# Optimization experiments

Hardware: AMD Instinct MI355X
Metric: run time of the kernel (lower is better)

Reference implementation:

```python
import jax, jax.numpy as jnp
import numpy as np

MARGIN = 0.2
NEG_INF = -1e9  # safe stand-in for -inf when masking the max


def setup_inputs() -> dict:
    key = jax.random.key(0)
    k1, k2, k3 = jax.random.split(key, 3)
    B, D = 8192, 256
    p = jax.random.normal(k1, (B, D), dtype=jnp.float32)
    # module docstring says projections are normalized
    projections = p / jnp.linalg.norm(p, axis=1, keepdims=True)
    affordance_ids = jax.random.randint(k2, (B,), 0, 36, dtype=jnp.int64)
    instance_ids = jax.random.randint(k3, (B,), 0, 2048, dtype=jnp.int64)
    return {
        "projections": projections,
        "affordance_ids": affordance_ids,
        "instance_ids": instance_ids,
    }


def reference(projections, affordance_ids, instance_ids):
    # (B, B) cosine similarities
    sim = jnp.matmul(projections, projections.T)

    aff_eq = affordance_ids[:, None] == affordance_ids[None, :]
    inst_eq = instance_ids[:, None] == instance_ids[None, :]
    pos_mask = aff_eq & ~inst_eq          # same affordance, different instance
    neg_mask = ~aff_eq                    # different affordance

    # per-row hard negative: max similarity over negatives
    hard_neg = jnp.max(jnp.where(neg_mask, sim, NEG_INF), axis=1)  # (B,)

    # rows contribute only if they have >=1 positive AND >=1 negative
    valid_row = pos_mask.any(axis=1) & neg_mask.any(axis=1)        # (B,)
    pair_mask = pos_mask & valid_row[:, None]                      # (B, B)

    # margin loss for every (anchor i, positive j) pair
    losses = jnp.maximum(hard_neg[:, None] - sim + MARGIN, 0.0)

    total = jnp.sum(jnp.where(pair_mask, losses, 0.0))
    num_pairs = jnp.sum(pair_mask)
    return jnp.where(num_pairs > 0, total / num_pairs, 0.0)
```

## Files before the change

kernel.cpp:

```cpp
#include <hip/hip_runtime.h>

#define NB 8192
#define ND 256
#define NCLS 64
#define LOSS_MARGIN 0.2f
#define NEG_INF_F (-1e9f)
#define LMAXT 3
#define NBLK_LOSS (NCLS * LMAXT * LMAXT)
#define NTILE_T 2080

typedef __attribute__((ext_vector_type(8))) __bf16 bf16x8;
typedef __attribute__((ext_vector_type(4))) float f32x4;

__device__ __forceinline__ unsigned f2u_mono(float f) {
  unsigned b = __float_as_uint(f);
  return (b & 0x80000000u) ? ~b : (b | 0x80000000u);
}
__device__ __forceinline__ float u2f_mono(unsigned u) {
  return (u & 0x80000000u) ? __uint_as_float(u & 0x7fffffffu)
                           : __uint_as_float(~u);
}

__device__ __forceinline__ unsigned short f2bf(float f) {
  unsigned u = __float_as_uint(f);
  unsigned r = (u + 0x7fffu + ((u >> 16) & 1u)) >> 16;
  return (unsigned short)r;
}

__device__ __forceinline__ void gl_lds16(const void* gsrc, void* ldst) {
  __builtin_amdgcn_global_load_lds(
      (const __attribute__((address_space(1))) void*)gsrc,
      (__attribute__((address_space(3))) void*)ldst, 16, 0, 0);
}

__global__ __launch_bounds__(1024) void build_idx_fused(const int* __restrict__ aff,
                                                        int* __restrict__ class_start,
                                                        int* __restrict__ class_idx) {
  const int c = blockIdx.x;
  const int t = threadIdx.x;
  const int lane = t & 63, wave = t >> 6;
  __shared__ int wtot[16];
  __shared__ int s_off;

  int lt = 0;
  for (int i = t; i < NB; i += 1024) lt += (aff[i] < c) ? 1 : 0;
  for (int off = 32; off; off >>= 1) lt += __shfl_down(lt, off);
  if (lane == 0) wtot[wave] = lt;
  __syncthreads();
  int base = 0;
  for (int w = 0; w < 16; ++w) base += wtot[w];
  if (t == 0) {
    class_start[c] = base;
    if (c == 0) class_start[NCLS] = NB;
  }
  __syncthreads();
  if (t == 0) s_off = 0;
  __syncthreads();

  for (int pass = 0; pass < NB / 1024; ++pass) {
    const int i = pass * 1024 + t;
    const bool m = (aff[i] == c);
    const unsigned long long mask = __ballot(m);
    if (lane == 0) wtot[wave] = __popcll(mask);
    __syncthreads();
    const int off = s_off;
    int prefix = 0;
    for (int w = 0; w < wave; ++w) prefix += wtot[w];
    if (m)
      class_idx[base + off + prefix +
                __popcll(mask & ((1ull << lane) - 1ull))] = i;
    __syncthreads();
    if (t == 0) {
      int tot = 0;
      for (int w = 0; w < 16; ++w) tot += wtot[w];
      s_off = off + tot;
    }
    __syncthreads();
  }
}

__global__ __launch_bounds__(256) void gather_convert(const float* __restrict__ P,
                                                      const int* __restrict__ aff,
                                                      const int* __restrict__ inst,
                                                      const int* __restrict__ class_idx,
                                                      unsigned short* __restrict__ Psort,
                                                      int* __restrict__ affSort,
                                                      int* __restrict__ instSort,
                                                      unsigned* __restrict__ hn_enc) {
  const int t = threadIdx.x;
  const int sr = blockIdx.x * 8 + (t >> 5);
  const int c = t & 31;
  const int src = class_idx[sr];
  const float4* ps = (const float4*)(P + (size_t)src * ND);
  ushort4* pd = (ushort4*)(Psort + (size_t)sr * ND);
#pragma unroll
  for (int q = 0; q < 2; ++q) {
    float4 v = ps[c + q * 32];
    ushort4 h;
    h.x = f2bf(v.x); h.y = f2bf(v.y); h.z = f2bf(v.z); h.w = f2bf(v.w);
    pd[c + q * 32] = h;
  }
  if (c == 0) {
    affSort[sr] = aff[src];
    instSort[sr] = inst[src];
    hn_enc[sr] = f2u_mono(NEG_INF_F);
  }
}

__global__ __launch_bounds__(256, 4) void simmax_mfma(const unsigned short* __restrict__ Psort,
                                                      const int* __restrict__ affSort,
                                                      unsigned* __restrict__ hn_enc) {
  int wg = blockIdx.x;
  wg = (wg & 7) * (NTILE_T / 8) + (wg >> 3);
  int bi = (int)((129.0f - sqrtf(129.0f * 129.0f - 8.0f * (float)wg)) * 0.5f);
  while (bi * 64 - bi * (bi - 1) / 2 > wg) --bi;
  while ((bi + 1) * 64 - (bi + 1) * bi / 2 <= wg) ++bi;
  const int bj = bi + (wg - (bi * 64 - bi * (bi - 1) / 2));

  __shared__ __align__(16) unsigned short At[2][4096];
  __shared__ __align__(16) unsigned short Bt[2][4096];
  __shared__ int affI[128], affJ[128];

  const int t = threadIdx.x;
  const int lane = t & 63;
  const int wave = t >> 6;
  const int r0 = bi * 128, c0 = bj * 128;

  if (t < 128) affI[t] = affSort[r0 + t];
  else affJ[t - 128] = affSort[c0 + (t - 128)];

  const int wr = (wave >> 1) * 64;
  const int wc = (wave & 1) * 64;

  f32x4 acc[4][4];
#pragma unroll
  for (int m = 0; m < 4; ++m)
#pragma unroll
    for (int n = 0; n < 4; ++n) acc[m][n] = (f32x4){0.f, 0.f, 0.f, 0.f};

  const int ci0 = t, ci1 = 256 + t;
  const int kg0 = ci0 >> 7, rw0 = ci0 & 127;
  const int kg1 = ci1 >> 7, rw1 = ci1 & 127;

#define STAGE_SIM(B, KC)                                                      \
  do {                                                                        \
    gl_lds16(Psort + (size_t)(r0 + rw0) * ND + (KC) + kg0 * 8, &At[B][ci0 * 8]); \
    gl_lds16(Psort + (size_t)(c0 + rw0) * ND + (KC) + kg0 * 8, &Bt[B][ci0 * 8]); \
    gl_lds16(Psort + (size_t)(r0 + rw1) * ND + (KC) + kg1 * 8, &At[B][ci1 * 8]); \
    gl_lds16(Psort + (size_t)(c0 + rw1) * ND + (KC) + kg1 * 8, &Bt[B][ci1 * 8]); \
  } while (0)

  STAGE_SIM(0, 0);
  asm volatile("s_waitcnt vmcnt(0) lgkmcnt(0)" ::: "memory");
  __builtin_amdgcn_s_barrier();
  __builtin_amdgcn_sched_barrier(0);

  int cur = 0;
#pragma unroll 1
  for (int s = 0; s < 8; ++s) {
    if (s < 7) STAGE_SIM(cur ^ 1, (s + 1) * 32);
    const int kg = lane >> 4, lr = lane & 15;
    bf16x8 a[4], b[4];
#pragma unroll
    for (int m = 0; m < 4; ++m)
      a[m] = *(const bf16x8*)&At[cur][(kg * 128 + wr + m * 16 + lr) * 8];
#pragma unroll
    for (int n = 0; n < 4; ++n)
      b[n] = *(const bf16x8*)&Bt[cur][(kg * 128 + wc + n * 16 + lr) * 8];
#pragma unroll
    for (int m = 0; m < 4; ++m)
#pragma unroll
      for (int n = 0; n < 4; ++n)
        acc[m][n] = __builtin_amdgcn_mfma_f32_16x16x32_bf16(a[m], b[n], acc[m][n], 0, 0, 0);
    __builtin_amdgcn_sched_barrier(0);
    if (s < 7) {
      asm volatile("s_waitcnt vmcnt(0) lgkmcnt(0)" ::: "memory");
      __builtin_amdgcn_s_barrier();
      __builtin_amdgcn_sched_barrier(0);
    }
    cur ^= 1;
  }

#pragma unroll
  for (int m = 0; m < 4; ++m) {
#pragma unroll
    for (int r = 0; r < 4; ++r) {
      const int lrow = wr + m * 16 + (lane >> 4) * 4 + r;
      const int ai = affI[lrow];
      float rmax = NEG_INF_F;
#pragma unroll
      for (int n = 0; n < 4; ++n) {
        const int lcol = wc + n * 16 + (lane & 15);
        if (affJ[lcol] != ai) rmax = fmaxf(rmax, acc[m][n][r]);
      }
      rmax = fmaxf(rmax, __shfl_xor(rmax, 1));
      rmax = fmaxf(rmax, __shfl_xor(rmax, 2));
      rmax = fmaxf(rmax, __shfl_xor(rmax, 4));
      rmax = fmaxf(rmax, __shfl_xor(rmax, 8));
      if ((lane & 15) == 0) atomicMax(&hn_enc[r0 + lrow], f2u_mono(rmax));
    }
  }
  if (bi != bj) {
#pragma unroll
    for (int n = 0; n < 4; ++n) {
      const int lcol = wc + n * 16 + (lane & 15);
      const int aj = affJ[lcol];
      float cmax = NEG_INF_F;
#pragma unroll
      for (int m = 0; m < 4; ++m) {
        const int lrb = wr + m * 16 + (lane >> 4) * 4;
#pragma unroll
        for (int r = 0; r < 4; ++r)
          if (affI[lrb + r] != aj) cmax = fmaxf(cmax, acc[m][n][r]);
      }
      cmax = fmaxf(cmax, __shfl_xor(cmax, 16));
      cmax = fmaxf(cmax, __shfl_xor(cmax, 32));
      if ((lane >> 4) == 0) atomicMax(&hn_enc[c0 + lcol], f2u_mono(cmax));
    }
  }
#undef STAGE_SIM
}

__global__ __launch_bounds__(256, 4) void loss_mfma(const unsigned short* __restrict__ Psort,
                                                    const int* __restrict__ class_start,
                                                    const int* __restrict__ instSort,
                                                    const unsigned* __restrict__ hn_enc,
                                                    float* __restrict__ bsum,
                                                    int* __restrict__ bcnt) {
  const int c = blockIdx.z;
  const int ti = blockIdx.x, tj = blockIdx.y;
  const int bid = (c * LMAXT + ti) * LMAXT + tj;
  const int t = threadIdx.x;
  const int base = class_start[c];
  const int cnt = class_start[c + 1] - base;
  const int nt = (cnt + 127) >> 7;
  if (ti >= nt || tj >= nt || cnt >= NB) {
    if (t == 0) { bsum[bid] = 0.f; bcnt[bid] = 0; }
    return;
  }

  __shared__ __align__(16) unsigned short At[2][4096];
  __shared__ __align__(16) unsigned short Bt[2][4096];
  __shared__ int instI[128], instJ[128];
  __shared__ float hnI[128];

  const int lane = t & 63;
  const int wave = t >> 6;

  if (t < 128) {
    int ri = ti * 128 + t;
    int gi = base + (ri < cnt ? ri : 0);
    instI[t] = instSort[gi];
    hnI[t] = u2f_mono(hn_enc[gi]);
  } else {
    int tt = t - 128;
    int rj = tj * 128 + tt;
    int gj = base + (rj < cnt ? rj : 0);
    instJ[tt] = instSort[gj];
  }

  const int wr = (wave >> 1) * 64;
  const int wc = (wave & 1) * 64;

  f32x4 acc[4][4];
#pragma unroll
  for (int m = 0; m < 4; ++m)
#pragma unroll
    for (int n = 0; n < 4; ++n) acc[m][n] = (f32x4){0.f, 0.f, 0.f, 0.f};

  const int ci0 = t, ci1 = 256 + t;
  const int kg0 = ci0 >> 7, rw0 = ci0 & 127;
  const int kg1 = ci1 >> 7, rw1 = ci1 & 127;
  const int ra0 = base + (ti * 128 + rw0 < cnt ? ti * 128 + rw0 : 0);
  const int ra1 = base + (ti * 128 + rw1 < cnt ? ti * 128 + rw1 : 0);
  const int rb0 = base + (tj * 128 + rw0 < cnt ? tj * 128 + rw0 : 0);
  const int rb1 = base + (tj * 128 + rw1 < cnt ? tj * 128 + rw1 : 0);

#define STAGE_LOSS(B, KC)                                               \
  do {                                                                  \
    gl_lds16(Psort + (size_t)ra0 * ND + (KC) + kg0 * 8, &At[B][ci0 * 8]); \
    gl_lds16(Psort + (size_t)rb0 * ND + (KC) + kg0 * 8, &Bt[B][ci0 * 8]); \
    gl_lds16(Psort + (size_t)ra1 * ND + (KC) + kg1 * 8, &At[B][ci1 * 8]); \
    gl_lds16(Psort + (size_t)rb1 * ND + (KC) + kg1 * 8, &Bt[B][ci1 * 8]); \
  } while (0)

  STAGE_LOSS(0, 0);
  asm volatile("s_waitcnt vmcnt(0) lgkmcnt(0)" ::: "memory");
  __builtin_amdgcn_s_barrier();
  __builtin_amdgcn_sched_barrier(0);

  int cur = 0;
#pragma unroll 1
  for (int s = 0; s < 8; ++s) {
    if (s < 7) STAGE_LOSS(cur ^ 1, (s + 1) * 32);
    const int kg = lane >> 4, lr = lane & 15;
    bf16x8 a[4], b[4];
#pragma unroll
    for (int m = 0; m < 4; ++m)
      a[m] = *(const bf16x8*)&At[cur][(kg * 128 + wr + m * 16 + lr) * 8];
#pragma unroll
    for (int n = 0; n < 4; ++n)
      b[n] = *(const bf16x8*)&Bt[cur][(kg * 128 + wc + n * 16 + lr) * 8];
#pragma unroll
    for (int m = 0; m < 4; ++m)
#pragma unroll
      for (int n = 0; n < 4; ++n)
        acc[m][n] = __builtin_amdgcn_mfma_f32_16x16x32_bf16(a[m], b[n], acc[m][n], 0, 0, 0);
    __builtin_amdgcn_sched_barrier(0);
    if (s < 7) {
      asm volatile("s_waitcnt vmcnt(0) lgkmcnt(0)" ::: "memory");
      __builtin_amdgcn_s_barrier();
      __builtin_amdgcn_sched_barrier(0);
    }
    cur ^= 1;
  }

  float lsum = 0.f;
  int lcnt = 0;
#pragma unroll
  for (int m = 0; m < 4; ++m) {
#pragma unroll
    for (int r = 0; r < 4; ++r) {
      const int lrow = wr + m * 16 + (lane >> 4) * 4 + r;
      const int ri = ti * 128 + lrow;
      if (ri >= cnt) continue;
      const float hn = hnI[lrow];
      const int ii = instI[lrow];
#pragma unroll
      for (int n = 0; n < 4; ++n) {
        const int lcol = wc + n * 16 + (lane & 15);
        const int rj = tj * 128 + lcol;
        if (rj < cnt && instJ[lcol] != ii) {
          lsum += fmaxf(hn - acc[m][n][r] + LOSS_MARGIN, 0.f);
          lcnt += 1;
        }
      }
    }
  }

  for (int off = 32; off; off >>= 1) {
    lsum += __shfl_down(lsum, off);
    lcnt += __shfl_down(lcnt, off);
  }
  __shared__ float wsum[4];
  __shared__ int wcnt[4];
  if (lane == 0) { wsum[wave] = lsum; wcnt[wave] = lcnt; }
  __syncthreads();
  if (t == 0) {
    bsum[bid] = wsum[0] + wsum[1] + wsum[2] + wsum[3];
    bcnt[bid] = wcnt[0] + wcnt[1] + wcnt[2] + wcnt[3];
  }
#undef STAGE_LOSS
}

__global__ __launch_bounds__(256) void finalize_kernel(const float* __restrict__ bsum,
                                                       const int* __restrict__ bcnt,
                                                       float* __restrict__ out) {
  const int t = threadIdx.x;
  float s = 0.f;
  int n = 0;
  for (int i = t; i < NBLK_LOSS; i += 256) { s += bsum[i]; n += bcnt[i]; }
  for (int off = 32; off; off >>= 1) {
    s += __shfl_down(s, off);
    n += __shfl_down(n, off);
  }
  __shared__ float wsum[4];
  __shared__ int wcnt[4];
  if ((t & 63) == 0) { wsum[t >> 6] = s; wcnt[t >> 6] = n; }
  __syncthreads();
  if (t == 0) {
    const float S = wsum[0] + wsum[1] + wsum[2] + wsum[3];
    const int N = wcnt[0] + wcnt[1] + wcnt[2] + wcnt[3];
    out[0] = (N > 0) ? (S / (float)N) : 0.0f;
  }
}

extern "C" void kernel_launch(void* const* d_in, const int* in_sizes, int n_in,
                              void* d_out, int out_size, void* d_ws, size_t ws_size,
                              hipStream_t stream) {
  const float* P = (const float*)d_in[0];
  const int* aff = (const int*)d_in[1];
  const int* inst = (const int*)d_in[2];
  float* out = (float*)d_out;

  unsigned short* Psort = (unsigned short*)d_ws;
  int* ibase = (int*)((char*)d_ws + (size_t)NB * ND * 2);
  unsigned* hn_enc = (unsigned*)ibase;
  int* class_start = ibase + NB;
  int* class_idx   = ibase + NB + NCLS + 1;
  int* affSort     = ibase + 2 * NB + NCLS + 1;
  int* instSort    = ibase + 3 * NB + NCLS + 1;
  float* bsum = (float*)(ibase + 4 * NB + NCLS + 1);
  int* bcnt   = ibase + 4 * NB + NCLS + 1 + NBLK_LOSS;

  build_idx_fused<<<NCLS, 1024, 0, stream>>>(aff, class_start, class_idx);
  gather_convert<<<NB / 8, 256, 0, stream>>>(P, aff, inst, class_idx, Psort,
                                             affSort, instSort, hn_enc);
  simmax_mfma<<<NTILE_T, 256, 0, stream>>>(Psort, affSort, hn_enc);
  loss_mfma<<<dim3(LMAXT, LMAXT, NCLS), 256, 0, stream>>>(Psort, class_start, instSort,
                                                          hn_enc, bsum, bcnt);
  finalize_kernel<<<1, 256, 0, stream>>>(bsum, bcnt, out);
}
```

Baseline: 103.6 us.

## Replace global atomicMax hard-negative reduction with per-tile partials and reduce kernel

Each sim tile now combines its row and column maxima through shared memory and writes them into a per-row partial array indexed by tile column. A new hn_reduce kernel takes the max over the 64 partials per row. This removes the global atomicMax traffic and the ordered-uint encoding/decoding. The cost is an extra kernel launch and 2 MB of partial writes and reads, plus one extra block barrier in the sim kernel.

```diff
diff --git a/kernel.cpp b/kernel.cpp
--- a/kernel.cpp
+++ b/kernel.cpp
@@ -11,15 +11,6 @@
 
 typedef __attribute__((ext_vector_type(8))) __bf16 bf16x8;
 typedef __attribute__((ext_vector_type(4))) float f32x4;
-
-__device__ __forceinline__ unsigned f2u_mono(float f) {
-  unsigned b = __float_as_uint(f);
-  return (b & 0x80000000u) ? ~b : (b | 0x80000000u);
-}
-__device__ __forceinline__ float u2f_mono(unsigned u) {
-  return (u & 0x80000000u) ? __uint_as_float(u & 0x7fffffffu)
-                           : __uint_as_float(~u);
-}
 
 __device__ __forceinline__ unsigned short f2bf(float f) {
   unsigned u = __float_as_uint(f);
@@ -85,8 +76,7 @@
                                                       const int* __restrict__ class_idx,
                                                       unsigned short* __restrict__ Psort,
                                                       int* __restrict__ affSort,
-                                                      int* __restrict__ instSort,
-                                                      unsigned* __restrict__ hn_enc) {
+                                                      int* __restrict__ instSort) {
   const int t = threadIdx.x;
   const int sr = blockIdx.x * 8 + (t >> 5);
   const int c = t & 31;
@@ -103,13 +93,12 @@
   if (c == 0) {
     affSort[sr] = aff[src];
     instSort[sr] = inst[src];
-    hn_enc[sr] = f2u_mono(NEG_INF_F);
   }
 }
 
 __global__ __launch_bounds__(256, 4) void simmax_mfma(const unsigned short* __restrict__ Psort,
                                                       const int* __restrict__ affSort,
-                                                      unsigned* __restrict__ hn_enc) {
+                                                      float* __restrict__ part) {
   int wg = blockIdx.x;
   wg = (wg & 7) * (NTILE_T / 8) + (wg >> 3);
   int bi = (int)((129.0f - sqrtf(129.0f * 129.0f - 8.0f * (float)wg)) * 0.5f);
@@ -120,6 +109,8 @@
   __shared__ __align__(16) unsigned short At[2][4096];
   __shared__ __align__(16) unsigned short Bt[2][4096];
   __shared__ int affI[128], affJ[128];
+  __shared__ float rowmax_s[128][2];
+  __shared__ float colmax_s[128][2];
 
   const int t = threadIdx.x;
   const int lane = t & 63;
@@ -197,7 +188,7 @@
       rmax = fmaxf(rmax, __shfl_xor(rmax, 2));
       rmax = fmaxf(rmax, __shfl_xor(rmax, 4));
       rmax = fmaxf(rmax, __shfl_xor(rmax, 8));
-      if ((lane & 15) == 0) atomicMax(&hn_enc[r0 + lrow], f2u_mono(rmax));
+      if ((lane & 15) == 0) rowmax_s[lrow][wc >> 6] = rmax;
     }
   }
   if (bi != bj) {
@@ -215,16 +206,36 @@
       }
       cmax = fmaxf(cmax, __shfl_xor(cmax, 16));
       cmax = fmaxf(cmax, __shfl_xor(cmax, 32));
-      if ((lane >> 4) == 0) atomicMax(&hn_enc[c0 + lcol], f2u_mono(cmax));
-    }
+      if (lane < 16) colmax_s[lcol][wr >> 6] = cmax;
+    }
+  }
+  __syncthreads();
+  if (t < 128) {
+    part[(size_t)(r0 + t) * 64 + bj] = fmaxf(rowmax_s[t][0], rowmax_s[t][1]);
+  } else if (bi != bj) {
+    const int c = t - 128;
+    part[(size_t)(c0 + c) * 64 + bi] = fmaxf(colmax_s[c][0], colmax_s[c][1]);
   }
 #undef STAGE_SIM
+}
+
+__global__ __launch_bounds__(256) void hn_reduce(const float* __restrict__ part,
+                                                 float* __restrict__ hn) {
+  const int i = blockIdx.x * 256 + threadIdx.x;
+  const float4* p = (const float4*)(part + (size_t)i * 64);
+  float m = NEG_INF_F;
+#pragma unroll
+  for (int q = 0; q < 16; ++q) {
+    float4 v = p[q];
+    m = fmaxf(m, fmaxf(fmaxf(v.x, v.y), fmaxf(v.z, v.w)));
+  }
+  hn[i] = m;
 }
 
 __global__ __launch_bounds__(256, 4) void loss_mfma(const unsigned short* __restrict__ Psort,
                                                     const int* __restrict__ class_start,
                                                     const int* __restrict__ instSort,
-                                                    const unsigned* __restrict__ hn_enc,
+                                                    const float* __restrict__ hn,
                                                     float* __restrict__ bsum,
                                                     int* __restrict__ bcnt) {
   const int c = blockIdx.z;
@@ -251,7 +262,7 @@
     int ri = ti * 128 + t;
     int gi = base + (ri < cnt ? ri : 0);
     instI[t] = instSort[gi];
-    hnI[t] = u2f_mono(hn_enc[gi]);
+    hnI[t] = hn[gi];
   } else {
     int tt = t - 128;
     int rj = tj * 128 + tt;
@@ -324,14 +335,14 @@
       const int lrow = wr + m * 16 + (lane >> 4) * 4 + r;
       const int ri = ti * 128 + lrow;
       if (ri >= cnt) continue;
-      const float hn = hnI[lrow];
+      const float hnv = hnI[lrow];
       const int ii = instI[lrow];
 #pragma unroll
       for (int n = 0; n < 4; ++n) {
         const int lcol = wc + n * 16 + (lane & 15);
         const int rj = tj * 128 + lcol;
         if (rj < cnt && instJ[lcol] != ii) {
-          lsum += fmaxf(hn - acc[m][n][r] + LOSS_MARGIN, 0.f);
+          lsum += fmaxf(hnv - acc[m][n][r] + LOSS_MARGIN, 0.f);
           lcnt += 1;
         }
       }
@@ -384,8 +395,9 @@
   float* out = (float*)d_out;
 
   unsigned short* Psort = (unsigned short*)d_ws;
-  int* ibase = (int*)((char*)d_ws + (size_t)NB * ND * 2);
-  unsigned* hn_enc = (unsigned*)ibase;
+  float* part = (float*)((char*)d_ws + (size_t)NB * ND * 2);
+  int* ibase = (int*)((char*)part + (size_t)NB * 64 * 4);
+  float* hn        = (float*)ibase;
   int* class_start = ibase + NB;
   int* class_idx   = ibase + NB + NCLS + 1;
   int* affSort     = ibase + 2 * NB + NCLS + 1;
@@ -395,9 +407,10 @@
 
   build_idx_fused<<<NCLS, 1024, 0, stream>>>(aff, class_start, class_idx);
   gather_convert<<<NB / 8, 256, 0, stream>>>(P, aff, inst, class_idx, Psort,
-                                             affSort, instSort, hn_enc);
-  simmax_mfma<<<NTILE_T, 256, 0, stream>>>(Psort, affSort, hn_enc);
+                                             affSort, instSort);
+  simmax_mfma<<<NTILE_T, 256, 0, stream>>>(Psort, affSort, part);
+  hn_reduce<<<NB / 256, 256, 0, stream>>>(part, hn);
   loss_mfma<<<dim3(LMAXT, LMAXT, NCLS), 256, 0, stream>>>(Psort, class_start, instSort,
-                                                          hn_enc, bsum, bcnt);
+                                                          hn, bsum, bcnt);
   finalize_kernel<<<1, 256, 0, stream>>>(bsum, bcnt, out);
 }
```

Result: faster. 90.62 us (-12.5%).
